# Kernel optimization log

Measured on AMD Instinct MI355X. Metric: run time of the kernel, lower is better.

Reference implementation:

```python
import jax, jax.numpy as jnp
import numpy as np

B = 1024           # number of jets (independent binary trees)
L = 10             # tree depth (levels); level j has B*2**j nodes
H = 128            # hidden size
FEAT = 7           # input features per node
LEVEL_SIZES = [B * 2**j for j in range(L)]
OFF = np.concatenate([[0], np.cumsum(LEVEL_SIZES)]).astype(int).tolist()
INNER = LEVEL_SIZES[:-1]                     # all non-bottom nodes are inner
COFF = np.concatenate([[0], np.cumsum(INNER)]).astype(int).tolist()


def _linear_init(key, fan_in, fan_out):
    return jax.random.normal(key, (fan_in, fan_out), jnp.float32) / np.sqrt(fan_in).astype(np.float32)


def setup_inputs() -> dict:
    key = jax.random.key(0)
    ks = jax.random.split(key, 6)
    contents = jax.random.normal(ks[0], (OFF[-1], FEAT), jnp.float32)
    # child indices are local to level j+1: node k at level j -> children (2k, 2k+1)
    ch = [np.stack([2 * np.arange(n), 2 * np.arange(n) + 1], axis=1) for n in INNER]
    children = jnp.asarray(np.concatenate(ch, axis=0), jnp.int32)
    return {
        "contents": contents,
        "children": children,
        "W_u": _linear_init(ks[1], FEAT, H), "b_u": jnp.zeros((H,), jnp.float32),
        "W_h": _linear_init(ks[2], 3 * H, H), "b_h": jnp.zeros((H,), jnp.float32),
        "W_z": _linear_init(ks[3], 4 * H, 4 * H), "b_z": jnp.zeros((4 * H,), jnp.float32),
        "W_r": _linear_init(ks[4], 3 * H, 3 * H), "b_r": jnp.zeros((3 * H,), jnp.float32),
        "conv_w": jnp.asarray([0.9], jnp.float32),
        "conv_b": jnp.asarray([0.01], jnp.float32),
    }


def reference(contents, children, W_u, b_u, W_h, b_h, W_z, b_z, W_r, b_r, conv_w, conv_b):
    def conv_chain(x):
        # relu(conv1x1(relu(conv1x1(relu(conv1x1(x)))))): Conv2d(1,1,1) == scalar scale + bias
        for _ in range(3):
            x = jax.nn.relu(conv_w[0] * x + conv_b[0])
        return x

    emb = None  # embeddings of the level below (level j+1)
    for j in reversed(range(L)):
        c = contents[OFF[j]:OFF[j + 1]]               # [N_j, FEAT]
        u = conv_chain(c @ W_u + b_u)                 # [N_j, H]
        if j == L - 1:                                # bottom level: all leaves
            emb = u
            continue
        ch = children[COFF[j]:COFF[j + 1]]            # [N_j, 2] indices into level j+1
        h_L = emb[ch[:, 0]]                           # gather left children
        h_R = emb[ch[:, 1]]                           # gather right children
        hhu = jnp.concatenate([h_L, h_R, u], axis=1)  # [N_j, 3H]
        r = jax.nn.sigmoid(hhu @ W_r + b_r)           # reset gate
        h_H = conv_chain((r * hhu) @ W_h + b_h)       # [N_j, H]
        z = jnp.concatenate([h_H, hhu], axis=1) @ W_z + b_z  # [N_j, 4H]
        g = jax.nn.softmax(
            jnp.stack([z[:, :H], z[:, H:2 * H], z[:, 2 * H:3 * H], z[:, 3 * H:]], axis=-1),
            axis=-1,
        )                                             # [N_j, H, 4] gate weights
        emb = g[..., 0] * h_H + g[..., 1] * h_L + g[..., 2] * h_R + g[..., 3] * u
    return emb.reshape(B, -1)                         # [B, H] root embeddings
```

## Files before the change

### kernel.cpp

```cpp
#include <hip/hip_runtime.h>
#include <hip/hip_bf16.h>

typedef _Float16 f16x8 __attribute__((ext_vector_type(8)));
typedef _Float16 f16x4 __attribute__((ext_vector_type(4)));
typedef float f32x4 __attribute__((ext_vector_type(4)));

#define H 128
#define FEAT 7
#define RB 64
#define NT 512

__device__ __forceinline__ float conv3(float x, float w, float b) {
    x = fmaxf(fmaf(w, x, b), 0.f);
    x = fmaxf(fmaf(w, x, b), 0.f);
    x = fmaxf(fmaf(w, x, b), 0.f);
    return x;
}
__device__ __forceinline__ float sigm(float x) {
    return __builtin_amdgcn_rcpf(1.f + __expf(-x));
}

__global__ __launch_bounds__(256) void pack_weights(
    const float* __restrict__ Wu, const float* __restrict__ Wr,
    const float* __restrict__ Wh, const float* __restrict__ Wz,
    _Float16* __restrict__ Pu, _Float16* __restrict__ Pr,
    _Float16* __restrict__ Ph, _Float16* __restrict__ Pz)
{
    int idx = blockIdx.x * 256 + threadIdx.x;
    if (idx < 384 * 384) {
        int k = idx / 384, n = idx % 384;
        Pr[((size_t)(k >> 3) * 384 + n) * 8 + (k & 7)] = (_Float16)Wr[idx];
    }
    if (idx < 384 * 128) {
        int k = idx / 128, n = idx % 128;
        Ph[((size_t)(k >> 3) * 128 + n) * 8 + (k & 7)] = (_Float16)Wh[idx];
    }
    if (idx < 512 * 512) {
        int k = idx / 512, n = idx % 512;
        Pz[((size_t)(k >> 3) * 512 + n) * 8 + (k & 7)] = (_Float16)Wz[idx];
    }
    if (idx < 128 * 32) {
        int n = idx & 127, kk = idx >> 7;
        Pu[((size_t)(kk >> 3) * 128 + n) * 8 + (kk & 7)] =
            (kk < FEAT) ? (_Float16)Wu[kk * H + n] : (_Float16)0.f;
    }
}

template<bool LEAF>
__global__ __launch_bounds__(NT, 2) void level_kernel(
    const float* __restrict__ contents,
    const int* __restrict__ children,
    const float* __restrict__ leafContents,
    const _Float16* __restrict__ embPrev,
    _Float16* __restrict__ embOut,
    float* __restrict__ finalOut,
    const _Float16* __restrict__ Pu, const float* __restrict__ bu,
    const _Float16* __restrict__ Pr, const float* __restrict__ br,
    const _Float16* __restrict__ Ph, const float* __restrict__ bh,
    const _Float16* __restrict__ Pz, const float* __restrict__ bz,
    const float* __restrict__ convw, const float* __restrict__ convb)
{
    __shared__ __align__(16) _Float16 s_hhu[RB][392];
    __shared__ __align__(16) _Float16 s_x[RB][392];
    __shared__ __align__(16) _Float16 s_hH[RB][136];

    const int t = threadIdx.x;
    const int row0 = blockIdx.x * RB;
    const float cw = convw[0], cbv = convb[0];

    const int lane = t & 63;
    const int w = t >> 6;
    const int q = lane >> 4;
    const int ln = lane & 15;

    const f16x8* PBc = (const f16x8*)Pr + (w * 48 + ln);
    f16x8 awc[3][3];
#pragma unroll
    for (int c = 0; c < 3; c++) awc[0][c] = PBc[(size_t)q * 384 + c * 16];
#pragma unroll
    for (int c = 0; c < 3; c++) awc[1][c] = PBc[(size_t)(4 + q) * 384 + c * 16];

    {
        _Float16* wbuf = (_Float16*)&s_x[0][0] + (size_t)w * 1536;
#pragma unroll
        for (int it = 0; it < 3; it++) {
            int r = it * 64 + lane;
            wbuf[r * 8 + 7] = (_Float16)0.f;
        }
#pragma unroll
        for (int it = 0; it < 7; it++) {
            int i = it * 64 + lane;
            float v = contents[(size_t)row0 * FEAT + i];
            int r = i / 7, k = i - r * 7;
            wbuf[r * 8 + k] = (_Float16)v;
        }
        if (LEAF) {
            int base = children[row0 * 2];
            const float* lc = leafContents + (size_t)base * FEAT;
#pragma unroll
            for (int it = 0; it < 14; it++) {
                int i = it * 64 + lane;
                float v = lc[i];
                int r = i / 7, k = i - r * 7;
                wbuf[512 + r * 8 + k] = (_Float16)v;
            }
        }
        f16x8 puF = ((const f16x8*)Pu)[(size_t)q * 128 + w * 16 + ln];
        const int fb = w * 16 + q * 4;
        f32x4 buv = *(const f32x4*)&bu[fb];
        {
            f16x8 bA[4];
#pragma unroll
            for (int rt = 0; rt < 4; rt++)
                bA[rt] = *(const f16x8*)&wbuf[(rt * 16 + ln) * 8];
            f32x4 accA[4];
#pragma unroll
            for (int rt = 0; rt < 4; rt++)
                accA[rt] = __builtin_amdgcn_mfma_f32_16x16x32_f16(puF, bA[rt], (f32x4){0,0,0,0}, 0, 0, 0);
#pragma unroll
            for (int rt = 0; rt < 4; rt++) {
                f16x4 hp;
#pragma unroll
                for (int reg = 0; reg < 4; reg++)
                    hp[reg] = (_Float16)conv3(accA[rt][reg] + buv[reg], cw, cbv);
                *(f16x4*)&s_hhu[rt * 16 + ln][256 + fb] = hp;
            }
        }
        if (LEAF) {
#pragma unroll
            for (int h = 0; h < 2; h++) {
                f16x8 bB[4];
#pragma unroll
                for (int rt = 0; rt < 4; rt++)
                    bB[rt] = *(const f16x8*)&wbuf[512 + ((h * 4 + rt) * 16 + ln) * 8];
                f32x4 accB[4];
#pragma unroll
                for (int rt = 0; rt < 4; rt++)
                    accB[rt] = __builtin_amdgcn_mfma_f32_16x16x32_f16(puF, bB[rt], (f32x4){0,0,0,0}, 0, 0, 0);
#pragma unroll
                for (int rt = 0; rt < 4; rt++) {
                    int rr = (h * 4 + rt) * 16 + ln;
                    f16x4 hp;
#pragma unroll
                    for (int reg = 0; reg < 4; reg++)
                        hp[reg] = (_Float16)conv3(accB[rt][reg] + buv[reg], cw, cbv);
                    *(f16x4*)&s_hhu[rr >> 1][(rr & 1) * 128 + fb] = hp;
                }
            }
        } else {
            int rp = t >> 4, chunk = t & 15;
#pragma unroll
            for (int p = 0; p < 4; p++) {
                int cr = p * 32 + rp;
                int child = children[row0 * 2 + cr];
                uint4 v = *(const uint4*)(embPrev + (size_t)child * H + chunk * 8);
                *(uint4*)&s_hhu[cr >> 1][(cr & 1) * 128 + chunk * 8] = v;
            }
        }
    }
    __syncthreads();

    const f16x8* PBd = (const f16x8*)Ph + (w * 16 + ln);
    f16x8 awd[3];

    {
        f32x4 acc[3][4];
#pragma unroll
        for (int c = 0; c < 3; c++)
#pragma unroll
            for (int rt = 0; rt < 4; rt++) acc[c][rt] = (f32x4){0,0,0,0};
        f16x8 bb[3][4];
#pragma unroll
        for (int rt = 0; rt < 4; rt++) bb[0][rt] = *(const f16x8*)&s_hhu[rt * 16 + ln][q * 8];
#pragma unroll
        for (int rt = 0; rt < 4; rt++) bb[1][rt] = *(const f16x8*)&s_hhu[rt * 16 + ln][32 + q * 8];
#pragma unroll
        for (int kk = 0; kk < 12; kk++) {
            if (kk + 2 < 12) {
                int kb = (kk + 2) * 4 + q;
#pragma unroll
                for (int c = 0; c < 3; c++) awc[(kk + 2) % 3][c] = PBc[(size_t)kb * 384 + c * 16];
#pragma unroll
                for (int rt = 0; rt < 4; rt++)
                    bb[(kk + 2) % 3][rt] = *(const f16x8*)&s_hhu[rt * 16 + ln][(kk + 2) * 32 + q * 8];
            }
#pragma unroll
            for (int c = 0; c < 3; c++)
#pragma unroll
                for (int rt = 0; rt < 4; rt++)
                    acc[c][rt] = __builtin_amdgcn_mfma_f32_16x16x32_f16(awc[kk % 3][c], bb[kk % 3][rt], acc[c][rt], 0, 0, 0);
        }
        awd[0] = PBd[(size_t)q * 128];
        awd[1] = PBd[(size_t)(4 + q) * 128];
#pragma unroll
        for (int c = 0; c < 3; c++) {
            int fb = w * 48 + c * 16 + q * 4;
            f32x4 bv = *(const f32x4*)&br[fb];
#pragma unroll
            for (int rt = 0; rt < 4; rt++) {
                int row = rt * 16 + ln;
                f16x4 hh = *(const f16x4*)&s_hhu[row][fb];
                f16x4 xv;
#pragma unroll
                for (int reg = 0; reg < 4; reg++) {
                    float rv = sigm(acc[c][rt][reg] + bv[reg]);
                    xv[reg] = (_Float16)(rv * (float)hh[reg]);
                }
                *(f16x4*)&s_x[row][fb] = xv;
            }
        }
    }
    __syncthreads();

    const f16x8* PBe = (const f16x8*)Pz + (w * 16 + ln);
    f16x8 awe[3][4];

    {
        f32x4 acc[4];
#pragma unroll
        for (int rt = 0; rt < 4; rt++) acc[rt] = (f32x4){0,0,0,0};
        f16x8 bb[3][4];
#pragma unroll
        for (int rt = 0; rt < 4; rt++) bb[0][rt] = *(const f16x8*)&s_x[rt * 16 + ln][q * 8];
#pragma unroll
        for (int rt = 0; rt < 4; rt++) bb[1][rt] = *(const f16x8*)&s_x[rt * 16 + ln][32 + q * 8];
#pragma unroll
        for (int kk = 0; kk < 12; kk++) {
            if (kk + 2 < 12) {
                int kb = (kk + 2) * 4 + q;
                awd[(kk + 2) % 3] = PBd[(size_t)kb * 128];
#pragma unroll
                for (int rt = 0; rt < 4; rt++)
                    bb[(kk + 2) % 3][rt] = *(const f16x8*)&s_x[rt * 16 + ln][(kk + 2) * 32 + q * 8];
            }
#pragma unroll
            for (int rt = 0; rt < 4; rt++)
                acc[rt] = __builtin_amdgcn_mfma_f32_16x16x32_f16(awd[kk % 3], bb[kk % 3][rt], acc[rt], 0, 0, 0);
        }
#pragma unroll
        for (int g = 0; g < 4; g++) awe[0][g] = PBe[(size_t)q * 512 + g * 128];
#pragma unroll
        for (int g = 0; g < 4; g++) awe[1][g] = PBe[(size_t)(4 + q) * 512 + g * 128];
        int fb = w * 16 + q * 4;
        f32x4 bhv = *(const f32x4*)&bh[fb];
#pragma unroll
        for (int rt = 0; rt < 4; rt++) {
            f16x4 hp;
#pragma unroll
            for (int reg = 0; reg < 4; reg++)
                hp[reg] = (_Float16)conv3(acc[rt][reg] + bhv[reg], cw, cbv);
            *(f16x4*)&s_hH[rt * 16 + ln][fb] = hp;
        }
    }
    __syncthreads();

    {
        const int nb = w * 16;
        f32x4 acc[4][4];
#pragma unroll
        for (int g = 0; g < 4; g++)
#pragma unroll
            for (int rt = 0; rt < 4; rt++) acc[g][rt] = (f32x4){0,0,0,0};
        f16x8 bb[3][4];
#pragma unroll
        for (int rt = 0; rt < 4; rt++) bb[0][rt] = *(const f16x8*)&s_hH[rt * 16 + ln][q * 8];
#pragma unroll
        for (int rt = 0; rt < 4; rt++) bb[1][rt] = *(const f16x8*)&s_hH[rt * 16 + ln][32 + q * 8];
#pragma unroll
        for (int kk = 0; kk < 16; kk++) {
            if (kk + 2 < 16) {
                int kb = (kk + 2) * 4 + q;
#pragma unroll
                for (int g = 0; g < 4; g++) awe[(kk + 2) % 3][g] = PBe[(size_t)kb * 512 + g * 128];
                if (kk + 2 < 4) {
#pragma unroll
                    for (int rt = 0; rt < 4; rt++)
                        bb[(kk + 2) % 3][rt] = *(const f16x8*)&s_hH[rt * 16 + ln][(kk + 2) * 32 + q * 8];
                } else {
                    int k0 = (kk + 2) * 32 - 128;
#pragma unroll
                    for (int rt = 0; rt < 4; rt++)
                        bb[(kk + 2) % 3][rt] = *(const f16x8*)&s_hhu[rt * 16 + ln][k0 + q * 8];
                }
            }
#pragma unroll
            for (int g = 0; g < 4; g++)
#pragma unroll
                for (int rt = 0; rt < 4; rt++)
                    acc[g][rt] = __builtin_amdgcn_mfma_f32_16x16x32_f16(awe[kk % 3][g], bb[kk % 3][rt], acc[g][rt], 0, 0, 0);
        }
        int colb = nb + q * 4;
        f32x4 bz0 = *(const f32x4*)&bz[colb];
        f32x4 bz1 = *(const f32x4*)&bz[128 + colb];
        f32x4 bz2 = *(const f32x4*)&bz[256 + colb];
        f32x4 bz3 = *(const f32x4*)&bz[384 + colb];
#pragma unroll
        for (int rt = 0; rt < 4; rt++) {
            int row = rt * 16 + ln;
            f16x4 hH4 = *(const f16x4*)&s_hH[row][colb];
            f16x4 hL4 = *(const f16x4*)&s_hhu[row][colb];
            f16x4 hR4 = *(const f16x4*)&s_hhu[row][128 + colb];
            f16x4 u4  = *(const f16x4*)&s_hhu[row][256 + colb];
            size_t gidx = (size_t)(row0 + row) * H + colb;
            if (finalOut) {
                f32x4 ov;
#pragma unroll
                for (int reg = 0; reg < 4; reg++) {
                    float z0 = acc[0][rt][reg] + bz0[reg];
                    float z1 = acc[1][rt][reg] + bz1[reg];
                    float z2 = acc[2][rt][reg] + bz2[reg];
                    float z3 = acc[3][rt][reg] + bz3[reg];
                    float m = fmaxf(fmaxf(z0, z1), fmaxf(z2, z3));
                    float e0 = __expf(z0 - m), e1 = __expf(z1 - m), e2 = __expf(z2 - m), e3 = __expf(z3 - m);
                    float inv = __builtin_amdgcn_rcpf(e0 + e1 + e2 + e3);
                    ov[reg] = (e0 * (float)hH4[reg] + e1 * (float)hL4[reg] +
                               e2 * (float)hR4[reg] + e3 * (float)u4[reg]) * inv;
                }
                *(f32x4*)&finalOut[gidx] = ov;
            } else {
                f16x4 ev;
#pragma unroll
                for (int reg = 0; reg < 4; reg++) {
                    float z0 = acc[0][rt][reg] + bz0[reg];
                    float z1 = acc[1][rt][reg] + bz1[reg];
                    float z2 = acc[2][rt][reg] + bz2[reg];
                    float z3 = acc[3][rt][reg] + bz3[reg];
                    float m = fmaxf(fmaxf(z0, z1), fmaxf(z2, z3));
                    float e0 = __expf(z0 - m), e1 = __expf(z1 - m), e2 = __expf(z2 - m), e3 = __expf(z3 - m);
                    float inv = __builtin_amdgcn_rcpf(e0 + e1 + e2 + e3);
                    ev[reg] = (_Float16)((e0 * (float)hH4[reg] + e1 * (float)hL4[reg] +
                                          e2 * (float)hR4[reg] + e3 * (float)u4[reg]) * inv);
                }
                *(f16x4*)&embOut[gidx] = ev;
            }
        }
    }
}

extern "C" void kernel_launch(void* const* d_in, const int* in_sizes, int n_in,
                              void* d_out, int out_size, void* d_ws, size_t ws_size,
                              hipStream_t stream) {
    const float* contents = (const float*)d_in[0];
    const int*   children = (const int*)d_in[1];
    const float* Wu = (const float*)d_in[2];
    const float* bu = (const float*)d_in[3];
    const float* Wh = (const float*)d_in[4];
    const float* bh = (const float*)d_in[5];
    const float* Wz = (const float*)d_in[6];
    const float* bz = (const float*)d_in[7];
    const float* Wr = (const float*)d_in[8];
    const float* br = (const float*)d_in[9];
    const float* convw = (const float*)d_in[10];
    const float* convb = (const float*)d_in[11];
    float* out = (float*)d_out;

    _Float16* Pr = (_Float16*)d_ws;
    _Float16* Ph = Pr + 384 * 384;
    _Float16* Pz = Ph + 384 * 128;
    _Float16* Pu = Pz + 512 * 512;
    _Float16* bufA = (_Float16*)((char*)d_ws + (1 << 20));
    _Float16* bufB = bufA + (size_t)262144 * H;

    auto OFFS = [](int j) -> long long { return 1024LL * ((1LL << j) - 1); };

    pack_weights<<<(512 * 512 + 255) / 256, 256, 0, stream>>>(Wu, Wr, Wh, Wz, Pu, Pr, Ph, Pz);

    {
        int n = 1024 << 8;
        level_kernel<true><<<n / RB, NT, 0, stream>>>(
            contents + OFFS(8) * FEAT, children + OFFS(8) * 2,
            contents + OFFS(9) * FEAT, nullptr, bufA, nullptr,
            Pu, bu, Pr, br, Ph, bh, Pz, bz, convw, convb);
    }

    _Float16* prev = bufA;
    _Float16* cur  = bufB;
    for (int j = 7; j >= 0; j--) {
        int n = 1024 << j;
        level_kernel<false><<<n / RB, NT, 0, stream>>>(
            contents + OFFS(j) * FEAT, children + OFFS(j) * 2,
            nullptr, prev, cur, (j == 0 ? out : nullptr),
            Pu, bu, Pr, br, Ph, bh, Pz, bz, convw, convb);
        _Float16* tmp = prev; prev = cur; cur = tmp;
    }
}
```

Measured before the change: 677.1 us.

## Switch GRU GEMMs from 16x16x32 to 32x32x16 MFMA tiles

Replaces the 16x16x32 f16 MFMA tiling, where each wave covered all 64 rows with four row tiles, with 32x32x16 MFMA tiles. Waves are now split into column groups and row halves, each covering 32 rows. This is meant to cut the LDS B-operand reads per MFMA and issue fewer, larger MFMA instructions. It relies on the packed weight layout matching the new lane indexing, which is not shown in the change, and it changes the accumulator register layout.

After: 855.9 us. 1.26x slower.

```diff
diff --git a/kernel.cpp b/kernel.cpp
--- a/kernel.cpp
+++ b/kernel.cpp
@@ -4,6 +4,7 @@
 typedef _Float16 f16x8 __attribute__((ext_vector_type(8)));
 typedef _Float16 f16x4 __attribute__((ext_vector_type(4)));
 typedef float f32x4 __attribute__((ext_vector_type(4)));
+typedef float f32x16 __attribute__((ext_vector_type(16)));
 
 #define H 128
 #define FEAT 7
@@ -73,12 +74,22 @@
     const int q = lane >> 4;
     const int ln = lane & 15;
 
-    const f16x8* PBc = (const f16x8*)Pr + (w * 48 + ln);
+    const int rn = lane & 31;
+    const int hi = lane >> 5;
+    const int cgrp = w & 3;
+    const int rt2 = w >> 2;
+    const int trow = rt2 * 32 + rn;
+
+    f32x16 zero16;
+#pragma unroll
+    for (int i = 0; i < 16; i++) zero16[i] = 0.f;
+
+    const f16x8* PBc = (const f16x8*)Pr + (size_t)hi * 384 + cgrp * 96 + rn;
     f16x8 awc[3][3];
 #pragma unroll
-    for (int c = 0; c < 3; c++) awc[0][c] = PBc[(size_t)q * 384 + c * 16];
-#pragma unroll
-    for (int c = 0; c < 3; c++) awc[1][c] = PBc[(size_t)(4 + q) * 384 + c * 16];
+    for (int c = 0; c < 3; c++) awc[0][c] = PBc[c * 32];
+#pragma unroll
+    for (int c = 0; c < 3; c++) awc[1][c] = PBc[768 + c * 32];
 
     {
         _Float16* wbuf = (_Float16*)&s_x[0][0] + (size_t)w * 1536;
@@ -160,176 +171,142 @@
     }
     __syncthreads();
 
-    const f16x8* PBd = (const f16x8*)Ph + (w * 16 + ln);
+    const f16x8* PBd = (const f16x8*)Ph + (size_t)hi * 128 + cgrp * 32 + rn;
     f16x8 awd[3];
 
     {
-        f32x4 acc[3][4];
-#pragma unroll
-        for (int c = 0; c < 3; c++)
-#pragma unroll
-            for (int rt = 0; rt < 4; rt++) acc[c][rt] = (f32x4){0,0,0,0};
-        f16x8 bb[3][4];
-#pragma unroll
-        for (int rt = 0; rt < 4; rt++) bb[0][rt] = *(const f16x8*)&s_hhu[rt * 16 + ln][q * 8];
-#pragma unroll
-        for (int rt = 0; rt < 4; rt++) bb[1][rt] = *(const f16x8*)&s_hhu[rt * 16 + ln][32 + q * 8];
-#pragma unroll
-        for (int kk = 0; kk < 12; kk++) {
-            if (kk + 2 < 12) {
-                int kb = (kk + 2) * 4 + q;
-#pragma unroll
-                for (int c = 0; c < 3; c++) awc[(kk + 2) % 3][c] = PBc[(size_t)kb * 384 + c * 16];
-#pragma unroll
-                for (int rt = 0; rt < 4; rt++)
-                    bb[(kk + 2) % 3][rt] = *(const f16x8*)&s_hhu[rt * 16 + ln][(kk + 2) * 32 + q * 8];
+        f32x16 acc[3];
+#pragma unroll
+        for (int c = 0; c < 3; c++) acc[c] = zero16;
+        f16x8 bb[3];
+        bb[0] = *(const f16x8*)&s_hhu[trow][hi * 8];
+        bb[1] = *(const f16x8*)&s_hhu[trow][16 + hi * 8];
+#pragma unroll
+        for (int ks = 0; ks < 24; ks++) {
+            if (ks + 2 < 24) {
+#pragma unroll
+                for (int c = 0; c < 3; c++) awc[(ks + 2) % 3][c] = PBc[(size_t)(ks + 2) * 768 + c * 32];
+                bb[(ks + 2) % 3] = *(const f16x8*)&s_hhu[trow][(ks + 2) * 16 + hi * 8];
             }
 #pragma unroll
             for (int c = 0; c < 3; c++)
-#pragma unroll
-                for (int rt = 0; rt < 4; rt++)
-                    acc[c][rt] = __builtin_amdgcn_mfma_f32_16x16x32_f16(awc[kk % 3][c], bb[kk % 3][rt], acc[c][rt], 0, 0, 0);
-        }
-        awd[0] = PBd[(size_t)q * 128];
-        awd[1] = PBd[(size_t)(4 + q) * 128];
+                acc[c] = __builtin_amdgcn_mfma_f32_32x32x16_f16(awc[ks % 3][c], bb[ks % 3], acc[c], 0, 0, 0);
+        }
+        awd[0] = PBd[0];
+        awd[1] = PBd[256];
 #pragma unroll
         for (int c = 0; c < 3; c++) {
-            int fb = w * 48 + c * 16 + q * 4;
-            f32x4 bv = *(const f32x4*)&br[fb];
-#pragma unroll
-            for (int rt = 0; rt < 4; rt++) {
-                int row = rt * 16 + ln;
-                f16x4 hh = *(const f16x4*)&s_hhu[row][fb];
+#pragma unroll
+            for (int p = 0; p < 4; p++) {
+                int fbase = cgrp * 96 + c * 32 + p * 8 + hi * 4;
+                f32x4 bv = *(const f32x4*)&br[fbase];
+                f16x4 hh = *(const f16x4*)&s_hhu[trow][fbase];
                 f16x4 xv;
 #pragma unroll
-                for (int reg = 0; reg < 4; reg++) {
-                    float rv = sigm(acc[c][rt][reg] + bv[reg]);
-                    xv[reg] = (_Float16)(rv * (float)hh[reg]);
+                for (int r = 0; r < 4; r++) {
+                    float rv = sigm(acc[c][p * 4 + r] + bv[r]);
+                    xv[r] = (_Float16)(rv * (float)hh[r]);
                 }
-                *(f16x4*)&s_x[row][fb] = xv;
+                *(f16x4*)&s_x[trow][fbase] = xv;
             }
         }
     }
     __syncthreads();
 
-    const f16x8* PBe = (const f16x8*)Pz + (w * 16 + ln);
+    const f16x8* PBe = (const f16x8*)Pz + (size_t)hi * 512 + cgrp * 32 + rn;
     f16x8 awe[3][4];
 
     {
-        f32x4 acc[4];
-#pragma unroll
-        for (int rt = 0; rt < 4; rt++) acc[rt] = (f32x4){0,0,0,0};
-        f16x8 bb[3][4];
-#pragma unroll
-        for (int rt = 0; rt < 4; rt++) bb[0][rt] = *(const f16x8*)&s_x[rt * 16 + ln][q * 8];
-#pragma unroll
-        for (int rt = 0; rt < 4; rt++) bb[1][rt] = *(const f16x8*)&s_x[rt * 16 + ln][32 + q * 8];
-#pragma unroll
-        for (int kk = 0; kk < 12; kk++) {
-            if (kk + 2 < 12) {
-                int kb = (kk + 2) * 4 + q;
-                awd[(kk + 2) % 3] = PBd[(size_t)kb * 128];
-#pragma unroll
-                for (int rt = 0; rt < 4; rt++)
-                    bb[(kk + 2) % 3][rt] = *(const f16x8*)&s_x[rt * 16 + ln][(kk + 2) * 32 + q * 8];
-            }
-#pragma unroll
-            for (int rt = 0; rt < 4; rt++)
-                acc[rt] = __builtin_amdgcn_mfma_f32_16x16x32_f16(awd[kk % 3], bb[kk % 3][rt], acc[rt], 0, 0, 0);
-        }
-#pragma unroll
-        for (int g = 0; g < 4; g++) awe[0][g] = PBe[(size_t)q * 512 + g * 128];
-#pragma unroll
-        for (int g = 0; g < 4; g++) awe[1][g] = PBe[(size_t)(4 + q) * 512 + g * 128];
-        int fb = w * 16 + q * 4;
-        f32x4 bhv = *(const f32x4*)&bh[fb];
-#pragma unroll
-        for (int rt = 0; rt < 4; rt++) {
+        f32x16 acc = zero16;
+        f16x8 bb[3];
+        bb[0] = *(const f16x8*)&s_x[trow][hi * 8];
+        bb[1] = *(const f16x8*)&s_x[trow][16 + hi * 8];
+#pragma unroll
+        for (int ks = 0; ks < 24; ks++) {
+            if (ks + 2 < 24) {
+                awd[(ks + 2) % 3] = PBd[(size_t)(ks + 2) * 256];
+                bb[(ks + 2) % 3] = *(const f16x8*)&s_x[trow][(ks + 2) * 16 + hi * 8];
+            }
+            acc = __builtin_amdgcn_mfma_f32_32x32x16_f16(awd[ks % 3], bb[ks % 3], acc, 0, 0, 0);
+        }
+#pragma unroll
+        for (int g = 0; g < 4; g++) awe[0][g] = PBe[g * 128];
+#pragma unroll
+        for (int g = 0; g < 4; g++) awe[1][g] = PBe[1024 + g * 128];
+#pragma unroll
+        for (int p = 0; p < 4; p++) {
+            int fbase = cgrp * 32 + p * 8 + hi * 4;
+            f32x4 bhv = *(const f32x4*)&bh[fbase];
             f16x4 hp;
 #pragma unroll
-            for (int reg = 0; reg < 4; reg++)
-                hp[reg] = (_Float16)conv3(acc[rt][reg] + bhv[reg], cw, cbv);
-            *(f16x4*)&s_hH[rt * 16 + ln][fb] = hp;
+            for (int r = 0; r < 4; r++)
+                hp[r] = (_Float16)conv3(acc[p * 4 + r] + bhv[r], cw, cbv);
+            *(f16x4*)&s_hH[trow][fbase] = hp;
         }
     }
     __syncthreads();
 
     {
-        const int nb = w * 16;
-        f32x4 acc[4][4];
-#pragma unroll
-        for (int g = 0; g < 4; g++)
-#pragma unroll
-            for (int rt = 0; rt < 4; rt++) acc[g][rt] = (f32x4){0,0,0,0};
-        f16x8 bb[3][4];
-#pragma unroll
-        for (int rt = 0; rt < 4; rt++) bb[0][rt] = *(const f16x8*)&s_hH[rt * 16 + ln][q * 8];
-#pragma unroll
-        for (int rt = 0; rt < 4; rt++) bb[1][rt] = *(const f16x8*)&s_hH[rt * 16 + ln][32 + q * 8];
-#pragma unroll
-        for (int kk = 0; kk < 16; kk++) {
-            if (kk + 2 < 16) {
-                int kb = (kk + 2) * 4 + q;
-#pragma unroll
-                for (int g = 0; g < 4; g++) awe[(kk + 2) % 3][g] = PBe[(size_t)kb * 512 + g * 128];
-                if (kk + 2 < 4) {
-#pragma unroll
-                    for (int rt = 0; rt < 4; rt++)
-                        bb[(kk + 2) % 3][rt] = *(const f16x8*)&s_hH[rt * 16 + ln][(kk + 2) * 32 + q * 8];
-                } else {
-                    int k0 = (kk + 2) * 32 - 128;
-#pragma unroll
-                    for (int rt = 0; rt < 4; rt++)
-                        bb[(kk + 2) % 3][rt] = *(const f16x8*)&s_hhu[rt * 16 + ln][k0 + q * 8];
-                }
+        f32x16 acc[4];
+#pragma unroll
+        for (int g = 0; g < 4; g++) acc[g] = zero16;
+        f16x8 bb[3];
+        bb[0] = *(const f16x8*)&s_hH[trow][hi * 8];
+        bb[1] = *(const f16x8*)&s_hH[trow][16 + hi * 8];
+#pragma unroll
+        for (int ks = 0; ks < 32; ks++) {
+            if (ks + 2 < 32) {
+#pragma unroll
+                for (int g = 0; g < 4; g++) awe[(ks + 2) % 3][g] = PBe[(size_t)(ks + 2) * 1024 + g * 128];
+                if (ks + 2 < 8)
+                    bb[(ks + 2) % 3] = *(const f16x8*)&s_hH[trow][(ks + 2) * 16 + hi * 8];
+                else
+                    bb[(ks + 2) % 3] = *(const f16x8*)&s_hhu[trow][(ks + 2) * 16 - 128 + hi * 8];
             }
 #pragma unroll
             for (int g = 0; g < 4; g++)
-#pragma unroll
-                for (int rt = 0; rt < 4; rt++)
-                    acc[g][rt] = __builtin_amdgcn_mfma_f32_16x16x32_f16(awe[kk % 3][g], bb[kk % 3][rt], acc[g][rt], 0, 0, 0);
-        }
-        int colb = nb + q * 4;
-        f32x4 bz0 = *(const f32x4*)&bz[colb];
-        f32x4 bz1 = *(const f32x4*)&bz[128 + colb];
-        f32x4 bz2 = *(const f32x4*)&bz[256 + colb];
-        f32x4 bz3 = *(const f32x4*)&bz[384 + colb];
-#pragma unroll
-        for (int rt = 0; rt < 4; rt++) {
-            int row = rt * 16 + ln;
-            f16x4 hH4 = *(const f16x4*)&s_hH[row][colb];
-            f16x4 hL4 = *(const f16x4*)&s_hhu[row][colb];
-            f16x4 hR4 = *(const f16x4*)&s_hhu[row][128 + colb];
-            f16x4 u4  = *(const f16x4*)&s_hhu[row][256 + colb];
-            size_t gidx = (size_t)(row0 + row) * H + colb;
+                acc[g] = __builtin_amdgcn_mfma_f32_32x32x16_f16(awe[ks % 3][g], bb[ks % 3], acc[g], 0, 0, 0);
+        }
+#pragma unroll
+        for (int p = 0; p < 4; p++) {
+            int colb = cgrp * 32 + p * 8 + hi * 4;
+            f32x4 bz0 = *(const f32x4*)&bz[colb];
+            f32x4 bz1 = *(const f32x4*)&bz[128 + colb];
+            f32x4 bz2 = *(const f32x4*)&bz[256 + colb];
+            f32x4 bz3 = *(const f32x4*)&bz[384 + colb];
+            f16x4 hH4 = *(const f16x4*)&s_hH[trow][colb];
+            f16x4 hL4 = *(const f16x4*)&s_hhu[trow][colb];
+            f16x4 hR4 = *(const f16x4*)&s_hhu[trow][128 + colb];
+            f16x4 u4  = *(const f16x4*)&s_hhu[trow][256 + colb];
+            size_t gidx = (size_t)(row0 + trow) * H + colb;
             if (finalOut) {
                 f32x4 ov;
 #pragma unroll
-                for (int reg = 0; reg < 4; reg++) {
-                    float z0 = acc[0][rt][reg] + bz0[reg];
-                    float z1 = acc[1][rt][reg] + bz1[reg];
-                    float z2 = acc[2][rt][reg] + bz2[reg];
-                    float z3 = acc[3][rt][reg] + bz3[reg];
+                for (int r = 0; r < 4; r++) {
+                    float z0 = acc[0][p * 4 + r] + bz0[r];
+                    float z1 = acc[1][p * 4 + r] + bz1[r];
+                    float z2 = acc[2][p * 4 + r] + bz2[r];
+                    float z3 = acc[3][p * 4 + r] + bz3[r];
                     float m = fmaxf(fmaxf(z0, z1), fmaxf(z2, z3));
                     float e0 = __expf(z0 - m), e1 = __expf(z1 - m), e2 = __expf(z2 - m), e3 = __expf(z3 - m);
                     float inv = __builtin_amdgcn_rcpf(e0 + e1 + e2 + e3);
-                    ov[reg] = (e0 * (float)hH4[reg] + e1 * (float)hL4[reg] +
-                               e2 * (float)hR4[reg] + e3 * (float)u4[reg]) * inv;
+                    ov[r] = (e0 * (float)hH4[r] + e1 * (float)hL4[r] +
+                             e2 * (float)hR4[r] + e3 * (float)u4[r]) * inv;
                 }
                 *(f32x4*)&finalOut[gidx] = ov;
             } else {
                 f16x4 ev;
 #pragma unroll
-                for (int reg = 0; reg < 4; reg++) {
-                    float z0 = acc[0][rt][reg] + bz0[reg];
-                    float z1 = acc[1][rt][reg] + bz1[reg];
-                    float z2 = acc[2][rt][reg] + bz2[reg];
-                    float z3 = acc[3][rt][reg] + bz3[reg];
+                for (int r = 0; r < 4; r++) {
+                    float z0 = acc[0][p * 4 + r] + bz0[r];
+                    float z1 = acc[1][p * 4 + r] + bz1[r];
+                    float z2 = acc[2][p * 4 + r] + bz2[r];
+                    float z3 = acc[3][p * 4 + r] + bz3[r];
                     float m = fmaxf(fmaxf(z0, z1), fmaxf(z2, z3));
                     float e0 = __expf(z0 - m), e1 = __expf(z1 - m), e2 = __expf(z2 - m), e3 = __expf(z3 - m);
                     float inv = __builtin_amdgcn_rcpf(e0 + e1 + e2 + e3);
-                    ev[reg] = (_Float16)((e0 * (float)hH4[reg] + e1 * (float)hL4[reg] +
-                                          e2 * (float)hR4[reg] + e3 * (float)u4[reg]) * inv);
+                    ev[r] = (_Float16)((e0 * (float)hH4[r] + e1 * (float)hL4[r] +
+                                        e2 * (float)hR4[r] + e3 * (float)u4[r]) * inv);
                 }
                 *(f16x4*)&embOut[gidx] = ev;
             }
```
